# Kernel optimization log

Hardware: AMD Instinct MI355X
Metric: run time of the kernel (lower is better)

The kernel has to match this reference:

```python
import jax, jax.numpy as jnp
import numpy as np

B = 4
NB = 8192   # points per batch
MB = 2048   # query points per batch
C_IN = 64
RADII = (0.2, 0.4)
NSAMPLES = (16, 32)
EPS = 1e-5


def setup_inputs() -> dict:
    key = jax.random.key(0)
    ks = jax.random.split(key, 8)
    inp = {}
    inp["xyz"] = jax.random.uniform(ks[0], (B * NB, 3), jnp.float32)
    inp["features"] = jax.random.normal(ks[1], (B * NB, C_IN), jnp.float32)
    inp["new_xyz"] = jax.random.uniform(ks[2], (B * MB, 3), jnp.float32)
    inp["xyz_batch_cnt"] = jnp.full((B,), NB, jnp.int32)
    inp["new_xyz_batch_cnt"] = jnp.full((B,), MB, jnp.int32)
    cin = C_IN + 3  # use_xyz=True concatenates relative xyz
    for s in range(2):
        k0, k1 = jax.random.split(ks[3 + s])
        inp[f"w{s}0"] = jax.random.normal(k0, (128, cin), jnp.float32) * (2.0 / cin) ** 0.5
        inp[f"g{s}0"] = jnp.ones((128,), jnp.float32)
        inp[f"b{s}0"] = jnp.zeros((128,), jnp.float32)
        inp[f"w{s}1"] = jax.random.normal(k1, (128, 128), jnp.float32) * (2.0 / 128) ** 0.5
        inp[f"g{s}1"] = jnp.ones((128,), jnp.float32)
        inp[f"b{s}1"] = jnp.zeros((128,), jnp.float32)
    return inp


def _ball_query(new_b, xyz_b, radius, nsample):
    # new_b: (B, M, 3), xyz_b: (B, N, 3)
    n = xyz_b.shape[1]
    # squared distances via the quadratic expansion (avoids (B,M,N,3) temp)
    d2 = (jnp.sum(new_b * new_b, -1)[:, :, None]
          + jnp.sum(xyz_b * xyz_b, -1)[:, None, :]
          - 2.0 * jnp.einsum('bmc,bnc->bmn', new_b, xyz_b))
    in_ball = d2 < radius * radius
    # first-nsample-in-original-order semantics of the CUDA ball query
    order_key = jnp.where(in_ball, jnp.arange(n, dtype=jnp.int32)[None, None, :], n)
    idxs = jnp.sort(order_key, axis=-1)[..., :nsample]        # (B, M, nsample)
    valid = idxs < n
    first = idxs[..., :1]                                     # pad with first found idx
    idx = jnp.where(valid, idxs, first)
    empty = ~valid[..., 0]                                    # no neighbor in ball
    idx = jnp.where(empty[..., None], 0, idx)
    return idx, empty


def _bn_relu(x, g, b):
    # training-mode BatchNorm2d over (M, nsample) per channel, then ReLU
    mean = jnp.mean(x, axis=(0, 1))
    var = jnp.var(x, axis=(0, 1))
    return jax.nn.relu((x - mean) * jax.lax.rsqrt(var + EPS) * g + b)


def _scale(xyz_b, feat_b, new_b, radius, nsample, w0, g0, b0, w1, g1, b1):
    idx, empty = _ball_query(new_b, xyz_b, radius, nsample)
    gather = jax.vmap(lambda pts, i: pts[i])                  # per-batch gather
    gx = gather(xyz_b, idx) - new_b[:, :, None, :]            # (B, M, ns, 3)
    gf = gather(feat_b, idx)                                  # (B, M, ns, C)
    g = jnp.concatenate([gx, gf], axis=-1)                    # use_xyz=True
    g = jnp.where(empty[..., None, None], 0.0, g)             # zero empty balls
    g = g.reshape(-1, nsample, g.shape[-1])                   # (M_total, ns, 3+C)
    h = _bn_relu(jnp.einsum('mnc,oc->mno', g, w0), g0, b0)    # shared 1x1 conv
    h = _bn_relu(jnp.einsum('mnc,oc->mno', h, w1), g1, b1)
    return jnp.max(h, axis=1)                                 # max_pool over ns


def reference(xyz, features, new_xyz, xyz_batch_cnt, new_xyz_batch_cnt,
              w00, g00, b00, w01, g01, b01,
              w10, g10, b10, w11, g11, b11):
    b = xyz_batch_cnt.shape[0]
    xyz_b = xyz.reshape(b, -1, 3)
    feat_b = features.reshape(b, -1, features.shape[-1])
    new_b = new_xyz.reshape(b, -1, 3)
    f0 = _scale(xyz_b, feat_b, new_b, RADII[0], NSAMPLES[0], w00, g00, b00, w01, g01, b01)
    f1 = _scale(xyz_b, feat_b, new_b, RADII[1], NSAMPLES[1], w10, g10, b10, w11, g11, b11)
    return new_xyz, jnp.concatenate([f0, f1], axis=1)         # (M_total, 256)
```

## Files before the change

### kernel.cpp

```cpp
#include <hip/hip_runtime.h>
#include <stdio.h>

#define NBP   8192
#define MTOT  8192
#define CIN   64
#define CO    128

#define EPR(...) do { fprintf(stderr, __VA_ARGS__); fflush(stderr); } while (0)

typedef short short8 __attribute__((ext_vector_type(8)));
typedef float floatx4 __attribute__((ext_vector_type(4)));
typedef unsigned short ushort;
typedef ushort ushort4v __attribute__((ext_vector_type(4)));

__device__ __forceinline__ ushort f2b(float f)
{
    union { unsigned int i; float f; } x; x.f = f;
    return (ushort)((x.i + 0x7fffu + ((x.i >> 16) & 1u)) >> 16);
}
__device__ __forceinline__ float b2f(ushort u)
{
    union { unsigned int i; float f; } x; x.i = ((unsigned int)u) << 16;
    return x.f;
}
__device__ __forceinline__ void split_rne(float v, ushort& h, ushort& l)
{
    ushort hh = f2b(v);
    h = hh; l = f2b(v - b2f(hh));
}

__global__ void __launch_bounds__(256, 1) StackSAModuleMSG_85761906966880_kernel(
    const float* __restrict__ xyz, const float* __restrict__ nxyz,
    float* __restrict__ out, float* __restrict__ stats,
    const float* __restrict__ feat, ushort* __restrict__ fh,
    int* __restrict__ idx0, int* __restrict__ idx1,
    int* __restrict__ empty0, int* __restrict__ empty1,
    const float* __restrict__ w00, const float* __restrict__ w01,
    const float* __restrict__ w10, const float* __restrict__ w11,
    ushort* __restrict__ wh00, ushort* __restrict__ wl00,
    ushort* __restrict__ wh01, ushort* __restrict__ wl01,
    ushort* __restrict__ wh10, ushort* __restrict__ wl10,
    ushort* __restrict__ wh11, ushort* __restrict__ wl11)
{
    if (blockIdx.x < MTOT/4) {
        const double r2a = 0.2 * 0.2;
        const double r2b = 0.4 * 0.4;
        int m    = blockIdx.x * 4 + (threadIdx.x >> 6);
        int lane = threadIdx.x & 63;
        int b    = m >> 11;
        int base = b * NBP;

        double nx = (double)nxyz[3*m+0];
        double ny = (double)nxyz[3*m+1];
        double nz = (double)nxyz[3*m+2];
        double nn = nx*nx + ny*ny + nz*nz;

        int cnt0 = 0, cnt1 = 0;
        int first0 = base, first1 = base;
        unsigned long long lt = (1ull << lane) - 1ull;

        for (int j = 0; j < NBP; j += 64) {
            int gi = base + j + lane;
            double px = (double)xyz[3*gi+0];
            double py = (double)xyz[3*gi+1];
            double pz = (double)xyz[3*gi+2];
            double pp = px*px + py*py + pz*pz;
            double dt = nx*px + ny*py + nz*pz;
            double d2 = nn + pp - 2.0*dt;
            bool in0 = d2 < r2a;
            bool in1 = d2 < r2b;
            unsigned long long m0 = __ballot(in0);
            unsigned long long m1 = __ballot(in1);
            if (in0) {
                int p0 = cnt0 + __popcll(m0 & lt);
                if (p0 < 16) idx0[m*16 + p0] = gi;
            }
            if (in1) {
                int p1 = cnt1 + __popcll(m1 & lt);
                if (p1 < 32) idx1[m*32 + p1] = gi;
            }
            if (cnt0 == 0 && m0) first0 = base + j + (__ffsll((long long)m0) - 1);
            if (cnt1 == 0 && m1) first1 = base + j + (__ffsll((long long)m1) - 1);
            cnt0 += __popcll(m0);
            cnt1 += __popcll(m1);
            if (cnt0 >= 16 && cnt1 >= 32) break;
        }
        int c0 = cnt0 < 16 ? cnt0 : 16;
        int c1 = cnt1 < 32 ? cnt1 : 32;
        if (lane >= c0 && lane < 16) idx0[m*16 + lane] = first0;
        if (lane >= c1 && lane < 32) idx1[m*32 + lane] = first1;
        if (lane == 0) { empty0[m] = (cnt0 == 0); empty1[m] = (cnt1 == 0); }
    } else {
        int i = (blockIdx.x - MTOT/4) * 256 + threadIdx.x;
        if (i < 1024) stats[i] = 0.f;
        if (i < MTOT*3) out[i] = nxyz[i];
        if (i < 128*128) {
            split_rne(w01[i], wh01[i], wl01[i]);
            split_rne(w11[i], wh11[i], wl11[i]);
        }
        if (i < 128*96) {
            int o = i / 96, kd = i - o*96;
            int c = (kd < 64) ? (kd + 3) : ((kd < 67) ? (kd - 64) : -1);
            float a = (c >= 0) ? w00[o*67 + c] : 0.f;
            split_rne(a, wh00[i], wl00[i]);
            float b = (c >= 0) ? w10[o*67 + c] : 0.f;
            split_rne(b, wh10[i], wl10[i]);
        }
        {
            float4 v = *(const float4*)(feat + (size_t)4*i);
            ushort4v h;
            h[0] = f2b(v.x); h[1] = f2b(v.y); h[2] = f2b(v.z); h[3] = f2b(v.w);
            *(ushort4v*)(fh + (size_t)4*i) = h;
        }
    }
}

template<int NS, int GM>
__device__ __forceinline__ void stats1_body(
    const ushort* __restrict__ fh,
    const float* __restrict__ xyz, const float* __restrict__ nxyz,
    const int* __restrict__ idx, const int* __restrict__ empty,
    const ushort* __restrict__ wh0, float* __restrict__ part,
    int bx, int t, ushort* ah)
{
    constexpr int ROWS = NS*GM;
    int m0 = bx * GM;
    int wv = t >> 6, lane = t & 63, l16 = lane & 15, qo = lane >> 4;
    int n0 = 32*wv;

    short8 bh[3][2];
#pragma unroll
    for (int ks = 0; ks < 3; ks++)
#pragma unroll
        for (int nt = 0; nt < 2; nt++)
            bh[ks][nt] = *(const short8*)(wh0 +
                (long long)(n0 + 16*nt + l16)*96 + ks*32 + qo*8);

    unsigned em = 0;
#pragma unroll
    for (int g = 0; g < GM; g++) em |= (empty[m0 + g] ? 1u : 0u) << g;
    const long long ib = (long long)m0 * NS;
    const short8 Z8 = {0,0,0,0,0,0,0,0};
#pragma unroll
    for (int e = t; e < ROWS*8; e += 256) {
        int n = e >> 3, c8 = e & 7;
        int gi = idx[ib + n];
        short8 v = *(const short8*)(fh + (size_t)gi*CIN + 8*c8);
        if ((em >> (n / NS)) & 1u) v = Z8;
        *(short8*)(ah + n*136 + 8*c8) = v;
    }
#pragma unroll
    for (int e = t; e < ROWS*4; e += 256) {
        int n = e >> 2, k3 = e & 3;
        short8 v = Z8;
        if (k3 == 0) {
            int g = n / NS;
            if (!((em >> g) & 1u)) {
                int gi = idx[ib + n];
#pragma unroll
                for (int c = 0; c < 3; c++)
                    v[c] = (short)f2b(xyz[3*gi+c] - nxyz[3*(m0+g)+c]);
            }
        }
        *(short8*)(ah + n*136 + 64 + 8*k3) = v;
    }
    __syncthreads();

    floatx4 acc[8][2];
#pragma unroll
    for (int i = 0; i < 8; i++) {
        acc[i][0] = (floatx4){0.f,0.f,0.f,0.f};
        acc[i][1] = (floatx4){0.f,0.f,0.f,0.f};
    }
#pragma unroll
    for (int ks = 0; ks < 3; ks++) {
        int kb = ks*32 + qo*8;
#pragma unroll
        for (int mt = 0; mt < 8; mt++) {
            int ao = (16*mt + l16)*136 + kb;
            short8 fh8 = *(const short8*)(ah + ao);
#pragma unroll
            for (int nt = 0; nt < 2; nt++)
                acc[mt][nt] = __builtin_amdgcn_mfma_f32_16x16x32_bf16(
                                  fh8, bh[ks][nt], acc[mt][nt], 0, 0, 0);
        }
    }

    float sum[2] = {0.f,0.f}, sq[2] = {0.f,0.f};
#pragma unroll
    for (int mt = 0; mt < 8; mt++)
#pragma unroll
        for (int nt = 0; nt < 2; nt++)
#pragma unroll
            for (int r = 0; r < 4; r++) {
                float a = acc[mt][nt][r];
                sum[nt] += a; sq[nt] = fmaf(a, a, sq[nt]);
            }
#pragma unroll
    for (int nt = 0; nt < 2; nt++) {
        sum[nt] += __shfl_xor(sum[nt], 16); sum[nt] += __shfl_xor(sum[nt], 32);
        sq[nt]  += __shfl_xor(sq[nt],  16); sq[nt]  += __shfl_xor(sq[nt],  32);
    }
    if (lane < 16) {
#pragma unroll
        for (int nt = 0; nt < 2; nt++) {
            int c = n0 + 16*nt + lane;
            part[(long long)bx*256 + c]       = sum[nt];
            part[(long long)bx*256 + 128 + c] = sq[nt];
        }
    }
}

__global__ void __launch_bounds__(256, 4) sa_stats1_both(
    const ushort* __restrict__ fh,
    const float* __restrict__ xyz, const float* __restrict__ nxyz,
    const int* __restrict__ idx0, const int* __restrict__ empty0,
    const ushort* __restrict__ wh00, float* __restrict__ partA,
    const int* __restrict__ idx1, const int* __restrict__ empty1,
    const ushort* __restrict__ wh10, float* __restrict__ partB)
{
    __shared__ ushort ah[128*136];
    int t = threadIdx.x;
    if (blockIdx.x < MTOT/8)
        stats1_body<16,8>(fh, xyz, nxyz, idx0, empty0, wh00, partA,
                          blockIdx.x, t, ah);
    else
        stats1_body<32,4>(fh, xyz, nxyz, idx1, empty1, wh10, partB,
                          blockIdx.x - MTOT/8, t, ah);
}

template<int NS, int GM>
__device__ __forceinline__ void fused_body(
    const ushort* __restrict__ fh,
    const float* __restrict__ xyz, const float* __restrict__ nxyz,
    const int* __restrict__ idx, const int* __restrict__ empty,
    const ushort* __restrict__ wh0, const ushort* __restrict__ wl0,
    const ushort* __restrict__ wh1, const ushort* __restrict__ wl1,
    const float* __restrict__ g0, const float* __restrict__ b0,
    const float* __restrict__ s1sum, const float* __restrict__ s1sq,
    float* __restrict__ part, float* __restrict__ mxo, float* __restrict__ mno,
    float invN, int bx, int t,
    ushort* ah, ushort* hb, float* kv, float* sv)
{
    const int TPG = NS/16;
    int m0 = bx * GM;
    int wv = t >> 6, lane = t & 63, l16 = lane & 15, qo = lane >> 4;
    int n0 = 32*wv;

    if (t < 128) {
        float mean = s1sum[t] * invN;
        float var  = s1sq[t] * invN - mean * mean;
        float k    = rsqrtf(var + 1e-5f) * g0[t];
        kv[t] = k;
        sv[t] = b0[t] - mean * k;
    }

    short8 b1h[3][2], b1l[3][2];
#pragma unroll
    for (int ks = 0; ks < 3; ks++)
#pragma unroll
        for (int nt = 0; nt < 2; nt++) {
            long long wo = (long long)(n0 + 16*nt + l16)*96 + ks*32 + qo*8;
            b1h[ks][nt] = *(const short8*)(wh0 + wo);
            b1l[ks][nt] = *(const short8*)(wl0 + wo);
        }

    unsigned em = 0;
#pragma unroll
    for (int g = 0; g < GM; g++) em |= (empty[m0 + g] ? 1u : 0u) << g;
    const long long ib = (long long)m0 * NS;
    int n1 = t >> 3, c8 = t & 7, n2 = n1 + 32;
    int n3 = t >> 2, k3 = t & 3;
    int gi1 = idx[ib + n1];
    int gi2 = idx[ib + n2];
    short8 vh1 = *(const short8*)(fh + (size_t)gi1*CIN + 8*c8);
    short8 vh2 = *(const short8*)(fh + (size_t)gi2*CIN + 8*c8);
    const short8 Z8 = {0,0,0,0,0,0,0,0};
    short8 vh3 = Z8;
    int g3 = n3 / NS;
    if (k3 == 0 && !((em >> g3) & 1u)) {
        int gi3 = idx[ib + n3];
#pragma unroll
        for (int c = 0; c < 3; c++)
            vh3[c] = (short)f2b(xyz[3*gi3+c] - nxyz[3*(m0+g3)+c]);
    }

    if ((em >> (n1 / NS)) & 1u) vh1 = Z8;
    if ((em >> (n2 / NS)) & 1u) vh2 = Z8;
    *(short8*)(ah + n1*136 + 8*c8) = vh1;
    *(short8*)(ah + n2*136 + 8*c8) = vh2;
    *(short8*)(ah + n3*136 + 64 + 8*k3) = vh3;
    __syncthreads();

    {
        floatx4 acc[4][2];
#pragma unroll
        for (int i = 0; i < 4; i++) {
            acc[i][0] = (floatx4){0.f,0.f,0.f,0.f};
            acc[i][1] = (floatx4){0.f,0.f,0.f,0.f};
        }
#pragma unroll
        for (int ks = 0; ks < 3; ks++) {
            int kb = ks*32 + qo*8;
#pragma unroll
            for (int mt = 0; mt < 4; mt++) {
                int ao = (16*mt + l16)*136 + kb;
                short8 fh8 = *(const short8*)(ah + ao);
#pragma unroll
                for (int nt = 0; nt < 2; nt++) {
                    acc[mt][nt] = __builtin_amdgcn_mfma_f32_16x16x32_bf16(
                                      fh8, b1l[ks][nt], acc[mt][nt], 0, 0, 0);
                    acc[mt][nt] = __builtin_amdgcn_mfma_f32_16x16x32_bf16(
                                      fh8, b1h[ks][nt], acc[mt][nt], 0, 0, 0);
                }
            }
        }

#pragma unroll
        for (int nt = 0; nt < 2; nt++) {
            int c = n0 + 16*nt + l16;
            float k = kv[c], s = sv[c];
#pragma unroll
            for (int mt = 0; mt < 4; mt++) {
                int rbase = 16*mt + qo*4;
#pragma unroll
                for (int r = 0; r < 4; r += 2) {
                    float h0 = fmaxf(fmaf(acc[mt][nt][r],   k, s), 0.f);
                    float h1 = fmaxf(fmaf(acc[mt][nt][r+1], k, s), 0.f);
                    unsigned int pk;
                    asm("v_cvt_pk_bf16_f32 %0, %1, %2"
                        : "=v"(pk) : "v"(h0), "v"(h1));
                    hb[(rbase + r    )*136 + c] = (ushort)(pk & 0xffffu);
                    hb[(rbase + r + 1)*136 + c] = (ushort)(pk >> 16);
                }
            }
        }

        short8 b2h[4][2], b2l[4][2];
#pragma unroll
        for (int ks = 0; ks < 4; ks++)
#pragma unroll
            for (int nt = 0; nt < 2; nt++) {
                long long wo = (long long)(n0 + 16*nt + l16)*128 + ks*32 + qo*8;
                b2h[ks][nt] = *(const short8*)(wh1 + wo);
                b2l[ks][nt] = *(const short8*)(wl1 + wo);
            }
        __syncthreads();

        floatx4 acc2[4][2];
#pragma unroll
        for (int i = 0; i < 4; i++) {
            acc2[i][0] = (floatx4){0.f,0.f,0.f,0.f};
            acc2[i][1] = (floatx4){0.f,0.f,0.f,0.f};
        }
#pragma unroll
        for (int ks = 0; ks < 4; ks++) {
            int kb = ks*32 + qo*8;
#pragma unroll
            for (int mt = 0; mt < 4; mt++) {
                int ao = (16*mt + l16)*136 + kb;
                short8 fh8 = *(const short8*)(hb + ao);
#pragma unroll
                for (int nt = 0; nt < 2; nt++) {
                    acc2[mt][nt] = __builtin_amdgcn_mfma_f32_16x16x32_bf16(
                                      fh8, b2l[ks][nt], acc2[mt][nt], 0, 0, 0);
                    acc2[mt][nt] = __builtin_amdgcn_mfma_f32_16x16x32_bf16(
                                      fh8, b2h[ks][nt], acc2[mt][nt], 0, 0, 0);
                }
            }
        }

        float sum[2] = {0.f,0.f}, sq[2] = {0.f,0.f};
        float Mx[GM][2], Mn[GM][2];
#pragma unroll
        for (int g = 0; g < GM; g++) {
            Mx[g][0] = -3.4e38f; Mx[g][1] = -3.4e38f;
            Mn[g][0] =  3.4e38f; Mn[g][1] =  3.4e38f;
        }
#pragma unroll
        for (int mt = 0; mt < 4; mt++) {
            int gg = mt / TPG;
#pragma unroll
            for (int nt = 0; nt < 2; nt++)
#pragma unroll
                for (int r = 0; r < 4; r++) {
                    float a = acc2[mt][nt][r];
                    sum[nt] += a; sq[nt] = fmaf(a, a, sq[nt]);
                    Mx[gg][nt] = fmaxf(Mx[gg][nt], a);
                    Mn[gg][nt] = fminf(Mn[gg][nt], a);
                }
        }
#pragma unroll
        for (int nt = 0; nt < 2; nt++) {
            sum[nt] += __shfl_xor(sum[nt], 16); sum[nt] += __shfl_xor(sum[nt], 32);
            sq[nt]  += __shfl_xor(sq[nt],  16); sq[nt]  += __shfl_xor(sq[nt],  32);
#pragma unroll
            for (int g = 0; g < GM; g++) {
                Mx[g][nt] = fmaxf(Mx[g][nt], __shfl_xor(Mx[g][nt], 16));
                Mx[g][nt] = fmaxf(Mx[g][nt], __shfl_xor(Mx[g][nt], 32));
                Mn[g][nt] = fminf(Mn[g][nt], __shfl_xor(Mn[g][nt], 16));
                Mn[g][nt] = fminf(Mn[g][nt], __shfl_xor(Mn[g][nt], 32));
            }
        }
        if (lane < 16) {
#pragma unroll
            for (int nt = 0; nt < 2; nt++) {
                int c = n0 + 16*nt + lane;
                part[(long long)bx*256 + c]       = sum[nt];
                part[(long long)bx*256 + 128 + c] = sq[nt];
#pragma unroll
                for (int g = 0; g < GM; g++) {
                    mxo[(long long)(m0+g)*128 + c] = Mx[g][nt];
                    mno[(long long)(m0+g)*128 + c] = Mn[g][nt];
                }
            }
        }
    }
}

__global__ void __launch_bounds__(256, 4) sa_fused_both(
    const ushort* __restrict__ fh,
    const float* __restrict__ xyz, const float* __restrict__ nxyz,
    const int* __restrict__ idx0, const int* __restrict__ empty0,
    const ushort* __restrict__ wh00, const ushort* __restrict__ wl00,
    const ushort* __restrict__ wh01, const ushort* __restrict__ wl01,
    const float* __restrict__ g00, const float* __restrict__ b00,
    const float* __restrict__ s1sumA, const float* __restrict__ s1sqA,
    float* __restrict__ partA, float* __restrict__ mx0, float* __restrict__ mn0,
    float invN0,
    const int* __restrict__ idx1, const int* __restrict__ empty1,
    const ushort* __restrict__ wh10, const ushort* __restrict__ wl10,
    const ushort* __restrict__ wh11, const ushort* __restrict__ wl11,
    const float* __restrict__ g10, const float* __restrict__ b10,
    const float* __restrict__ s1sumB, const float* __restrict__ s1sqB,
    float* __restrict__ partB, float* __restrict__ mx1, float* __restrict__ mn1,
    float invN1)
{
    __shared__ ushort ah[64*136];
    __shared__ ushort hb[64*136];
    __shared__ float kv[128], sv[128];
    int t = threadIdx.x;
    if (blockIdx.x < MTOT/4)
        fused_body<16,4>(fh, xyz, nxyz, idx0, empty0,
                         wh00, wl00, wh01, wl01, g00, b00, s1sumA, s1sqA,
                         partA, mx0, mn0, invN0, blockIdx.x, t,
                         ah, hb, kv, sv);
    else
        fused_body<32,2>(fh, xyz, nxyz, idx1, empty1,
                         wh10, wl10, wh11, wl11, g10, b10, s1sumB, s1sqB,
                         partB, mx1, mn1, invN1, blockIdx.x - MTOT/4, t,
                         ah, hb, kv, sv);
}

__global__ void __launch_bounds__(256, 1) sa_reduce2(
    const float* __restrict__ partA, int nbA, float* __restrict__ dstA,
    const float* __restrict__ partB, int nbB, float* __restrict__ dstB)
{
    __shared__ float red[256];
    int t = threadIdx.x;
    const float* part; float* dst; int nb, b;
    if (blockIdx.x < 256) { part = partA; dst = dstA; nb = nbA; b = blockIdx.x; }
    else                  { part = partB; dst = dstB; nb = nbB; b = blockIdx.x - 256; }
    float s = 0.f;
    for (int i = t; i < nb; i += 256) s += part[(long long)i*256 + b];
    red[t] = s;
    __syncthreads();
    for (int off = 128; off > 0; off >>= 1) {
        if (t < off) red[t] += red[t + off];
        __syncthreads();
    }
    if (t == 0) dst[b] = red[0];
}

__global__ void __launch_bounds__(256, 1) sa_pass3b(
    const float* __restrict__ mx0, const float* __restrict__ mn0,
    const float* __restrict__ g01, const float* __restrict__ b01,
    const float* __restrict__ mx1, const float* __restrict__ mn1,
    const float* __restrict__ g11, const float* __restrict__ b11,
    const float* __restrict__ stats, float* __restrict__ outp,
    float invN0, float invN1)
{
    int i = blockIdx.x * 256 + threadIdx.x;
    int m = i >> 8, o = i & 255;
    bool sc1 = o >= 128;
    int oc = o & 127;
    const float* sm = sc1 ? (stats + 768) : (stats + 256);
    const float* sp = sc1 ? (stats + 896) : (stats + 384);
    float invN = sc1 ? invN1 : invN0;
    float gg   = sc1 ? g11[oc] : g01[oc];
    float bb   = sc1 ? b11[oc] : b01[oc];
    float mean = sm[oc] * invN;
    float var  = sp[oc] * invN - mean * mean;
    float k    = rsqrtf(var + 1e-5f) * gg;
    float sh   = bb - mean * k;
    long long mi = (long long)m * 128 + oc;
    float v;
    if (k >= 0.f) v = sc1 ? mx1[mi] : mx0[mi];
    else          v = sc1 ? mn1[mi] : mn0[mi];
    float r = fmaf(v, k, sh);
    outp[i] = r > 0.f ? r : 0.f;
}

extern "C" void kernel_launch(void* const* d_in, const int* in_sizes, int n_in,
                              void* d_out, int out_size, void* d_ws, size_t ws_size,
                              hipStream_t stream)
{
    const float* xyz  = (const float*)d_in[0];
    const float* feat = (const float*)d_in[1];
    const float* nxyz = (const float*)d_in[2];
    const float* w00 = (const float*)d_in[5];
    const float* g00 = (const float*)d_in[6];
    const float* b00 = (const float*)d_in[7];
    const float* w01 = (const float*)d_in[8];
    const float* g01 = (const float*)d_in[9];
    const float* b01 = (const float*)d_in[10];
    const float* w10 = (const float*)d_in[11];
    const float* g10 = (const float*)d_in[12];
    const float* b10 = (const float*)d_in[13];
    const float* w11 = (const float*)d_in[14];
    const float* g11 = (const float*)d_in[15];
    const float* b11 = (const float*)d_in[16];
    float* out = (float*)d_out;

    char*  wsb    = (char*)d_ws;
    float* stats  = (float*)(wsb);
    int*   idx0   = (int*)(wsb + 4096);
    int*   idx1   = (int*)(wsb + 4096 + 524288);
    int*   empty0 = (int*)(wsb + 4096 + 524288 + 1048576);
    int*   empty1 = (int*)(wsb + 4096 + 524288 + 1048576 + 32768);
    ushort* fh    = (ushort*)(wsb + 2000000);
    float* mx0    = (float*)(wsb + 150000000);
    float* mn0    = (float*)(wsb + 155000000);
    float* mx1    = (float*)(wsb + 160000000);
    float* mn1    = (float*)(wsb + 165000000);
    ushort* wh01  = (ushort*)(wsb + 170000000);
    ushort* wl01  = (ushort*)(wsb + 171000000);
    ushort* wh11  = (ushort*)(wsb + 172000000);
    ushort* wl11  = (ushort*)(wsb + 173000000);
    ushort* wh00  = (ushort*)(wsb + 174000000);
    ushort* wl00  = (ushort*)(wsb + 175000000);
    ushort* wh10  = (ushort*)(wsb + 176000000);
    ushort* wl10  = (ushort*)(wsb + 177000000);
    float* partA  = (float*)(wsb + 180000000);
    float* partB  = (float*)(wsb + 183000000);

    const float invN0 = 1.0f / (float)(MTOT*16);
    const float invN1 = 1.0f / (float)(MTOT*32);
    float* fout = out + MTOT*3;

    StackSAModuleMSG_85761906966880_kernel<<<MTOT/4 + 2048, 256, 0, stream>>>(
        xyz, nxyz, out, stats, feat, fh,
        idx0, idx1, empty0, empty1,
        w00, w01, w10, w11,
        wh00, wl00, wh01, wl01, wh10, wl10, wh11, wl11);

    sa_stats1_both<<<MTOT/8 + MTOT/4, 256, 0, stream>>>(
        fh, xyz, nxyz,
        idx0, empty0, wh00, partA,
        idx1, empty1, wh10, partB);

    sa_reduce2<<<512, 256, 0, stream>>>(partA, MTOT/8, stats + 0,
                                        partB, MTOT/4, stats + 512);

    sa_fused_both<<<MTOT/4 + MTOT/2, 256, 0, stream>>>(
        fh, xyz, nxyz,
        idx0, empty0, wh00, wl00, wh01, wl01, g00, b00,
        stats + 0, stats + 128, partA, mx0, mn0, invN0,
        idx1, empty1, wh10, wl10, wh11, wl11, g10, b10,
        stats + 512, stats + 640, partB, mx1, mn1, invN1);

    sa_reduce2<<<512, 256, 0, stream>>>(partA, MTOT/4, stats + 256,
                                        partB, MTOT/2, stats + 768);

    sa_pass3b<<<(MTOT*256)/256, 256, 0, stream>>>(
        mx0, mn0, g01, b01, mx1, mn1, g11, b11, stats, fout, invN0, invN1);

    hipError_t e = hipGetLastError();
    if (e != hipSuccess) EPR("[KL] enqueue err=%d (%s)\n", (int)e, hipGetErrorString(e));
}
```

Baseline: 232.0 us.

## Reuse one LDS tile for both layers and stream weights in double-buffered registers

The fused MLP kernel drops the second shared-memory tile and writes the layer-1 activations back into the input tile, adding a barrier so all reads finish before the overwrite. Weight fragments for both 1x1 convs now sit in a two-slot register buffer that is reloaded between k-steps instead of all being held at once, and the two accumulator sets are merged into one. This lowers LDS use and VGPR pressure so more blocks can share a CU. The cost is an extra barrier and global weight loads placed between the MFMA groups, which can expose load latency.

```diff
diff --git a/kernel.cpp b/kernel.cpp
--- a/kernel.cpp
+++ b/kernel.cpp
@@ -240,7 +240,7 @@
     const float* __restrict__ s1sum, const float* __restrict__ s1sq,
     float* __restrict__ part, float* __restrict__ mxo, float* __restrict__ mno,
     float invN, int bx, int t,
-    ushort* ah, ushort* hb, float* kv, float* sv)
+    ushort* ah, float* kv, float* sv)
 {
     const int TPG = NS/16;
     int m0 = bx * GM;
@@ -255,15 +255,18 @@
         sv[t] = b0[t] - mean * k;
     }
 
-    short8 b1h[3][2], b1l[3][2];
-#pragma unroll
-    for (int ks = 0; ks < 3; ks++)
-#pragma unroll
-        for (int nt = 0; nt < 2; nt++) {
-            long long wo = (long long)(n0 + 16*nt + l16)*96 + ks*32 + qo*8;
-            b1h[ks][nt] = *(const short8*)(wh0 + wo);
-            b1l[ks][nt] = *(const short8*)(wl0 + wo);
-        }
+    const long long wrow0 = (long long)(n0 + l16);
+    const long long wrow1 = (long long)(n0 + 16 + l16);
+
+    short8 wsh[2][2], wsl[2][2];
+
+#pragma unroll
+    for (int ks = 0; ks < 2; ks++) {
+        wsh[ks][0] = *(const short8*)(wh0 + wrow0*96 + ks*32 + qo*8);
+        wsl[ks][0] = *(const short8*)(wl0 + wrow0*96 + ks*32 + qo*8);
+        wsh[ks][1] = *(const short8*)(wh0 + wrow1*96 + ks*32 + qo*8);
+        wsl[ks][1] = *(const short8*)(wl0 + wrow1*96 + ks*32 + qo*8);
+    }
 
     unsigned em = 0;
 #pragma unroll
@@ -292,127 +295,182 @@
     *(short8*)(ah + n3*136 + 64 + 8*k3) = vh3;
     __syncthreads();
 
-    {
-        floatx4 acc[4][2];
-#pragma unroll
-        for (int i = 0; i < 4; i++) {
-            acc[i][0] = (floatx4){0.f,0.f,0.f,0.f};
-            acc[i][1] = (floatx4){0.f,0.f,0.f,0.f};
-        }
-#pragma unroll
-        for (int ks = 0; ks < 3; ks++) {
-            int kb = ks*32 + qo*8;
-#pragma unroll
-            for (int mt = 0; mt < 4; mt++) {
-                int ao = (16*mt + l16)*136 + kb;
-                short8 fh8 = *(const short8*)(ah + ao);
-#pragma unroll
-                for (int nt = 0; nt < 2; nt++) {
-                    acc[mt][nt] = __builtin_amdgcn_mfma_f32_16x16x32_bf16(
-                                      fh8, b1l[ks][nt], acc[mt][nt], 0, 0, 0);
-                    acc[mt][nt] = __builtin_amdgcn_mfma_f32_16x16x32_bf16(
-                                      fh8, b1h[ks][nt], acc[mt][nt], 0, 0, 0);
-                }
+    floatx4 acc[4][2];
+#pragma unroll
+    for (int i = 0; i < 4; i++) {
+        acc[i][0] = (floatx4){0.f,0.f,0.f,0.f};
+        acc[i][1] = (floatx4){0.f,0.f,0.f,0.f};
+    }
+
+#pragma unroll
+    for (int mt = 0; mt < 4; mt++) {
+        short8 fh8 = *(const short8*)(ah + (16*mt + l16)*136 + qo*8);
+#pragma unroll
+        for (int nt = 0; nt < 2; nt++) {
+            acc[mt][nt] = __builtin_amdgcn_mfma_f32_16x16x32_bf16(
+                              fh8, wsl[0][nt], acc[mt][nt], 0, 0, 0);
+            acc[mt][nt] = __builtin_amdgcn_mfma_f32_16x16x32_bf16(
+                              fh8, wsh[0][nt], acc[mt][nt], 0, 0, 0);
+        }
+    }
+    wsh[0][0] = *(const short8*)(wh0 + wrow0*96 + 64 + qo*8);
+    wsl[0][0] = *(const short8*)(wl0 + wrow0*96 + 64 + qo*8);
+    wsh[0][1] = *(const short8*)(wh0 + wrow1*96 + 64 + qo*8);
+    wsl[0][1] = *(const short8*)(wl0 + wrow1*96 + 64 + qo*8);
+#pragma unroll
+    for (int mt = 0; mt < 4; mt++) {
+        short8 fh8 = *(const short8*)(ah + (16*mt + l16)*136 + 32 + qo*8);
+#pragma unroll
+        for (int nt = 0; nt < 2; nt++) {
+            acc[mt][nt] = __builtin_amdgcn_mfma_f32_16x16x32_bf16(
+                              fh8, wsl[1][nt], acc[mt][nt], 0, 0, 0);
+            acc[mt][nt] = __builtin_amdgcn_mfma_f32_16x16x32_bf16(
+                              fh8, wsh[1][nt], acc[mt][nt], 0, 0, 0);
+        }
+    }
+#pragma unroll
+    for (int mt = 0; mt < 4; mt++) {
+        short8 fh8 = *(const short8*)(ah + (16*mt + l16)*136 + 64 + qo*8);
+#pragma unroll
+        for (int nt = 0; nt < 2; nt++) {
+            acc[mt][nt] = __builtin_amdgcn_mfma_f32_16x16x32_bf16(
+                              fh8, wsl[0][nt], acc[mt][nt], 0, 0, 0);
+            acc[mt][nt] = __builtin_amdgcn_mfma_f32_16x16x32_bf16(
+                              fh8, wsh[0][nt], acc[mt][nt], 0, 0, 0);
+        }
+    }
+
+    __syncthreads();
+
+#pragma unroll
+    for (int nt = 0; nt < 2; nt++) {
+        int c = n0 + 16*nt + l16;
+        float k = kv[c], s = sv[c];
+#pragma unroll
+        for (int mt = 0; mt < 4; mt++) {
+            int rbase = 16*mt + qo*4;
+#pragma unroll
+            for (int r = 0; r < 4; r += 2) {
+                float h0 = fmaxf(fmaf(acc[mt][nt][r],   k, s), 0.f);
+                float h1 = fmaxf(fmaf(acc[mt][nt][r+1], k, s), 0.f);
+                unsigned int pk;
+                asm("v_cvt_pk_bf16_f32 %0, %1, %2"
+                    : "=v"(pk) : "v"(h0), "v"(h1));
+                ah[(rbase + r    )*136 + c] = (ushort)(pk & 0xffffu);
+                ah[(rbase + r + 1)*136 + c] = (ushort)(pk >> 16);
             }
         }
-
-#pragma unroll
-        for (int nt = 0; nt < 2; nt++) {
-            int c = n0 + 16*nt + l16;
-            float k = kv[c], s = sv[c];
-#pragma unroll
-            for (int mt = 0; mt < 4; mt++) {
-                int rbase = 16*mt + qo*4;
-#pragma unroll
-                for (int r = 0; r < 4; r += 2) {
-                    float h0 = fmaxf(fmaf(acc[mt][nt][r],   k, s), 0.f);
-                    float h1 = fmaxf(fmaf(acc[mt][nt][r+1], k, s), 0.f);
-                    unsigned int pk;
-                    asm("v_cvt_pk_bf16_f32 %0, %1, %2"
-                        : "=v"(pk) : "v"(h0), "v"(h1));
-                    hb[(rbase + r    )*136 + c] = (ushort)(pk & 0xffffu);
-                    hb[(rbase + r + 1)*136 + c] = (ushort)(pk >> 16);
-                }
+    }
+
+#pragma unroll
+    for (int ks = 0; ks < 2; ks++) {
+        wsh[ks][0] = *(const short8*)(wh1 + wrow0*128 + ks*32 + qo*8);
+        wsl[ks][0] = *(const short8*)(wl1 + wrow0*128 + ks*32 + qo*8);
+        wsh[ks][1] = *(const short8*)(wh1 + wrow1*128 + ks*32 + qo*8);
+        wsl[ks][1] = *(const short8*)(wl1 + wrow1*128 + ks*32 + qo*8);
+    }
+    __syncthreads();
+
+#pragma unroll
+    for (int i = 0; i < 4; i++) {
+        acc[i][0] = (floatx4){0.f,0.f,0.f,0.f};
+        acc[i][1] = (floatx4){0.f,0.f,0.f,0.f};
+    }
+#pragma unroll
+    for (int mt = 0; mt < 4; mt++) {
+        short8 fh8 = *(const short8*)(ah + (16*mt + l16)*136 + qo*8);
+#pragma unroll
+        for (int nt = 0; nt < 2; nt++) {
+            acc[mt][nt] = __builtin_amdgcn_mfma_f32_16x16x32_bf16(
+                              fh8, wsl[0][nt], acc[mt][nt], 0, 0, 0);
+            acc[mt][nt] = __builtin_amdgcn_mfma_f32_16x16x32_bf16(
+                              fh8, wsh[0][nt], acc[mt][nt], 0, 0, 0);
+        }
+    }
+    wsh[0][0] = *(const short8*)(wh1 + wrow0*128 + 64 + qo*8);
+    wsl[0][0] = *(const short8*)(wl1 + wrow0*128 + 64 + qo*8);
+    wsh[0][1] = *(const short8*)(wh1 + wrow1*128 + 64 + qo*8);
+    wsl[0][1] = *(const short8*)(wl1 + wrow1*128 + 64 + qo*8);
+#pragma unroll
+    for (int mt = 0; mt < 4; mt++) {
+        short8 fh8 = *(const short8*)(ah + (16*mt + l16)*136 + 32 + qo*8);
+#pragma unroll
+        for (int nt = 0; nt < 2; nt++) {
+            acc[mt][nt] = __builtin_amdgcn_mfma_f32_16x16x32_bf16(
+                              fh8, wsl[1][nt], acc[mt][nt], 0, 0, 0);
+            acc[mt][nt] = __builtin_amdgcn_mfma_f32_16x16x32_bf16(
+                              fh8, wsh[1][nt], acc[mt][nt], 0, 0, 0);
+        }
+    }
+    wsh[1][0] = *(const short8*)(wh1 + wrow0*128 + 96 + qo*8);
+    wsl[1][0] = *(const short8*)(wl1 + wrow0*128 + 96 + qo*8);
+    wsh[1][1] = *(const short8*)(wh1 + wrow1*128 + 96 + qo*8);
+    wsl[1][1] = *(const short8*)(wl1 + wrow1*128 + 96 + qo*8);
+#pragma unroll
+    for (int mt = 0; mt < 4; mt++) {
+        short8 fh8 = *(const short8*)(ah + (16*mt + l16)*136 + 64 + qo*8);
+#pragma unroll
+        for (int nt = 0; nt < 2; nt++) {
+            acc[mt][nt] = __builtin_amdgcn_mfma_f32_16x16x32_bf16(
+                              fh8, wsl[0][nt], acc[mt][nt], 0, 0, 0);
+            acc[mt][nt] = __builtin_amdgcn_mfma_f32_16x16x32_bf16(
+                              fh8, wsh[0][nt], acc[mt][nt], 0, 0, 0);
+        }
+    }
+#pragma unroll
+    for (int mt = 0; mt < 4; mt++) {
+        short8 fh8 = *(const short8*)(ah + (16*mt + l16)*136 + 96 + qo*8);
+#pragma unroll
+        for (int nt = 0; nt < 2; nt++) {
+            acc[mt][nt] = __builtin_amdgcn_mfma_f32_16x16x32_bf16(
+                              fh8, wsl[1][nt], acc[mt][nt], 0, 0, 0);
+            acc[mt][nt] = __builtin_amdgcn_mfma_f32_16x16x32_bf16(
+                              fh8, wsh[1][nt], acc[mt][nt], 0, 0, 0);
+        }
+    }
+
+    float sum[2] = {0.f,0.f}, sq[2] = {0.f,0.f};
+    float Mx[GM][2], Mn[GM][2];
+#pragma unroll
+    for (int g = 0; g < GM; g++) {
+        Mx[g][0] = -3.4e38f; Mx[g][1] = -3.4e38f;
+        Mn[g][0] =  3.4e38f; Mn[g][1] =  3.4e38f;
+    }
+#pragma unroll
+    for (int mt = 0; mt < 4; mt++) {
+        int gg = mt / TPG;
+#pragma unroll
+        for (int nt = 0; nt < 2; nt++)
+#pragma unroll
+            for (int r = 0; r < 4; r++) {
+                float a = acc[mt][nt][r];
+                sum[nt] += a; sq[nt] = fmaf(a, a, sq[nt]);
+                Mx[gg][nt] = fmaxf(Mx[gg][nt], a);
+                Mn[gg][nt] = fminf(Mn[gg][nt], a);
             }
-        }
-
-        short8 b2h[4][2], b2l[4][2];
-#pragma unroll
-        for (int ks = 0; ks < 4; ks++)
-#pragma unroll
-            for (int nt = 0; nt < 2; nt++) {
-                long long wo = (long long)(n0 + 16*nt + l16)*128 + ks*32 + qo*8;
-                b2h[ks][nt] = *(const short8*)(wh1 + wo);
-                b2l[ks][nt] = *(const short8*)(wl1 + wo);
-            }
-        __syncthreads();
-
-        floatx4 acc2[4][2];
-#pragma unroll
-        for (int i = 0; i < 4; i++) {
-            acc2[i][0] = (floatx4){0.f,0.f,0.f,0.f};
-            acc2[i][1] = (floatx4){0.f,0.f,0.f,0.f};
-        }
-#pragma unroll
-        for (int ks = 0; ks < 4; ks++) {
-            int kb = ks*32 + qo*8;
-#pragma unroll
-            for (int mt = 0; mt < 4; mt++) {
-                int ao = (16*mt + l16)*136 + kb;
-                short8 fh8 = *(const short8*)(hb + ao);
-#pragma unroll
-                for (int nt = 0; nt < 2; nt++) {
-                    acc2[mt][nt] = __builtin_amdgcn_mfma_f32_16x16x32_bf16(
-                                      fh8, b2l[ks][nt], acc2[mt][nt], 0, 0, 0);
-                    acc2[mt][nt] = __builtin_amdgcn_mfma_f32_16x16x32_bf16(
-                                      fh8, b2h[ks][nt], acc2[mt][nt], 0, 0, 0);
-                }
-            }
-        }
-
-        float sum[2] = {0.f,0.f}, sq[2] = {0.f,0.f};
-        float Mx[GM][2], Mn[GM][2];
+    }
+#pragma unroll
+    for (int nt = 0; nt < 2; nt++) {
+        sum[nt] += __shfl_xor(sum[nt], 16); sum[nt] += __shfl_xor(sum[nt], 32);
+        sq[nt]  += __shfl_xor(sq[nt],  16); sq[nt]  += __shfl_xor(sq[nt],  32);
 #pragma unroll
         for (int g = 0; g < GM; g++) {
-            Mx[g][0] = -3.4e38f; Mx[g][1] = -3.4e38f;
-            Mn[g][0] =  3.4e38f; Mn[g][1] =  3.4e38f;
-        }
-#pragma unroll
-        for (int mt = 0; mt < 4; mt++) {
-            int gg = mt / TPG;
-#pragma unroll
-            for (int nt = 0; nt < 2; nt++)
-#pragma unroll
-                for (int r = 0; r < 4; r++) {
-                    float a = acc2[mt][nt][r];
-                    sum[nt] += a; sq[nt] = fmaf(a, a, sq[nt]);
-                    Mx[gg][nt] = fmaxf(Mx[gg][nt], a);
-                    Mn[gg][nt] = fminf(Mn[gg][nt], a);
-                }
-        }
-#pragma unroll
-        for (int nt = 0; nt < 2; nt++) {
-            sum[nt] += __shfl_xor(sum[nt], 16); sum[nt] += __shfl_xor(sum[nt], 32);
-            sq[nt]  += __shfl_xor(sq[nt],  16); sq[nt]  += __shfl_xor(sq[nt],  32);
+            Mx[g][nt] = fmaxf(Mx[g][nt], __shfl_xor(Mx[g][nt], 16));
+            Mx[g][nt] = fmaxf(Mx[g][nt], __shfl_xor(Mx[g][nt], 32));
+            Mn[g][nt] = fminf(Mn[g][nt], __shfl_xor(Mn[g][nt], 16));
+            Mn[g][nt] = fminf(Mn[g][nt], __shfl_xor(Mn[g][nt], 32));
+        }
+    }
+    if (lane < 16) {
+#pragma unroll
+        for (int nt = 0; nt < 2; nt++) {
+            int c = n0 + 16*nt + lane;
+            part[(long long)bx*256 + c]       = sum[nt];
+            part[(long long)bx*256 + 128 + c] = sq[nt];
 #pragma unroll
             for (int g = 0; g < GM; g++) {
-                Mx[g][nt] = fmaxf(Mx[g][nt], __shfl_xor(Mx[g][nt], 16));
-                Mx[g][nt] = fmaxf(Mx[g][nt], __shfl_xor(Mx[g][nt], 32));
-                Mn[g][nt] = fminf(Mn[g][nt], __shfl_xor(Mn[g][nt], 16));
-                Mn[g][nt] = fminf(Mn[g][nt], __shfl_xor(Mn[g][nt], 32));
-            }
-        }
-        if (lane < 16) {
-#pragma unroll
-            for (int nt = 0; nt < 2; nt++) {
-                int c = n0 + 16*nt + lane;
-                part[(long long)bx*256 + c]       = sum[nt];
-                part[(long long)bx*256 + 128 + c] = sq[nt];
-#pragma unroll
-                for (int g = 0; g < GM; g++) {
-                    mxo[(long long)(m0+g)*128 + c] = Mx[g][nt];
-                    mno[(long long)(m0+g)*128 + c] = Mn[g][nt];
-                }
+                mxo[(long long)(m0+g)*128 + c] = Mx[g][nt];
+                mno[(long long)(m0+g)*128 + c] = Mn[g][nt];
             }
         }
     }
@@ -437,19 +495,18 @@
     float invN1)
 {
     __shared__ ushort ah[64*136];
-    __shared__ ushort hb[64*136];
     __shared__ float kv[128], sv[128];
     int t = threadIdx.x;
     if (blockIdx.x < MTOT/4)
         fused_body<16,4>(fh, xyz, nxyz, idx0, empty0,
                          wh00, wl00, wh01, wl01, g00, b00, s1sumA, s1sqA,
                          partA, mx0, mn0, invN0, blockIdx.x, t,
-                         ah, hb, kv, sv);
+                         ah, kv, sv);
     else
         fused_body<32,2>(fh, xyz, nxyz, idx1, empty1,
                          wh10, wl10, wh11, wl11, g10, b10, s1sumB, s1sqB,
                          partB, mx1, mn1, invN1, blockIdx.x - MTOT/4, t,
-                         ah, hb, kv, sv);
+                         ah, kv, sv);
 }
 
 __global__ void __launch_bounds__(256, 1) sa_reduce2(
```

After: 234.3 us. Within noise of the previous version (+1.0%).
